# Kernel optimization log

Hardware: AMD Instinct MI355X
Metric: run time of the kernel (lower is better)

The kernel has to match this reference:

```python
import math
import jax, jax.numpy as jnp
import numpy as np

B, H, W, C = 2, 32, 32, 64
K = 15
G = 4
GC = C // G
K2 = K * K
RED = C // 4
MAX_SIGMA = 0.5


def setup_inputs() -> dict:
    key = jax.random.key(0)
    ks = jax.random.split(key, 32)
    f32 = jnp.float32

    def rn(k, shape, std):
        return (jax.random.normal(k, shape) * std).astype(f32)

    lin = 1.0 / math.sqrt(C)
    inp = {
        'x': jax.random.normal(ks[0], (B, H, W, C), f32),
        'raw_sigma': jnp.asarray(math.log(math.exp(0.3) - 1.0), f32),
        'base_offset_scale': jnp.asarray(0.1, f32),
        # input/output projections (stored [in,out])
        'w_ip': rn(ks[1], (C, C), lin), 'b_ip': jnp.zeros((C,), f32),
        'w_op': rn(ks[2], (C, C), lin), 'b_op': jnp.zeros((C,), f32),
        # dw_conv: depthwise 3x3 (HWIO, I=1) then pointwise 1x1 ([in,out])
        'w_dw': rn(ks[3], (3, 3, 1, C), 1.0 / 3.0), 'b_dw': jnp.zeros((C,), f32),
        'w_pw': rn(ks[4], (C, C), lin), 'b_pw': jnp.zeros((C,), f32),
        # offset / mask heads (original zero-inits; small random to exercise path)
        'w_off': rn(ks[5], (C, G * K2 * 2), 0.01), 'b_off': rn(ks[6], (G * K2 * 2,), 0.01),
        'w_msk': rn(ks[7], (C, G * K2), 0.01), 'b_msk': rn(ks[8], (G * K2,), 0.01),
        # kernel MLP: 2 -> 32 -> 32 -> G*GC
        'w_k1': rn(ks[9], (2, 32), 0.5), 'b_k1': jnp.zeros((32,), f32),
        'w_k2': rn(ks[10], (32, 32), 1.0 / math.sqrt(32)), 'b_k2': jnp.zeros((32,), f32),
        'w_k3': rn(ks[11], (32, G * GC), 1.0 / math.sqrt(32)), 'b_k3': jnp.zeros((G * GC,), f32),
        # SE block
        'w_fc1': rn(ks[12], (C, RED), lin), 'b_fc1': jnp.zeros((RED,), f32),
        'w_fc2': rn(ks[13], (RED, C), 1.0 / math.sqrt(RED)), 'b_fc2': jnp.zeros((C,), f32),
    }
    return inp


def _forward(x, raw_sigma, base_offset_scale, w_ip, b_ip, w_op, b_op, w_dw, b_dw,
             w_pw, b_pw, w_off, b_off, w_msk, b_msk, w_k1, b_k1, w_k2, b_k2,
             w_k3, b_k3, w_fc1, b_fc1, w_fc2, b_fc2):
    Bx, Hx, Wx, Cx = x.shape
    sigma = jnp.clip(jax.nn.softplus(raw_sigma), 1e-3, MAX_SIGMA)
    grid = jnp.linspace(-0.5, 0.5, K)  # [K]

    x_proj = x @ w_ip + b_ip  # [B,H,W,C]

    # depthwise 3x3 (SAME) + SiLU + pointwise 1x1
    y = jax.lax.conv_general_dilated(
        x, w_dw, (1, 1), 'SAME',
        dimension_numbers=('NHWC', 'HWIO', 'NHWC'), feature_group_count=Cx) + b_dw
    x_dw = jax.nn.silu(y) @ w_pw + b_pw  # [B,H,W,C]

    # Gaussian envelope over kernel grid, normalized
    env = jnp.exp(-(grid[:, None] ** 2 + grid[None, :] ** 2) / (2.0 * sigma ** 2))
    env = env / jnp.maximum(env.sum(), 1e-8)
    env_flat = env.reshape(1, 1, 1, 1, K2)

    gh, gw = jnp.meshgrid(grid, grid, indexing='ij')
    pos = jnp.stack([gh.ravel(), gw.ravel()], axis=-1) * 2.0  # [K2,2]
    hkw = jax.nn.silu(pos @ w_k1 + b_k1)
    hkw = jax.nn.silu(hkw @ w_k2 + b_k2)
    kw_raw = hkw @ w_k3 + b_k3  # [K2, G*GC]
    # faithful to torch view quirk: (K,K,G,gc) memory reinterpreted as (G,K2,gc)
    kw = kw_raw.reshape(G, K2, GC).reshape(1, 1, 1, G, K2, GC)

    offsets = (x_dw @ w_off + b_off).reshape(Bx, Hx, Wx, G, K2, 2) * base_offset_scale
    raw_mask = (x_dw @ w_msk + b_msk).reshape(Bx, Hx, Wx, G, K2) * env_flat
    attn = jnp.nan_to_num(jax.nn.softmax(raw_mask, axis=-1))

    # absolute sampling locations
    ref = jnp.linspace(-(K // 2), K // 2, K)
    rh, rw = jnp.meshgrid(ref, ref, indexing='ij')  # [K,K]
    pos_h = jnp.arange(Hx, dtype=x.dtype).reshape(1, Hx, 1, 1, 1)
    pos_w = jnp.arange(Wx, dtype=x.dtype).reshape(1, 1, Wx, 1, 1)
    abs_h = pos_h + rh.ravel().reshape(1, 1, 1, 1, K2) + offsets[..., 0]
    abs_w = pos_w + rw.ravel().reshape(1, 1, 1, 1, K2) + offsets[..., 1]
    ah = jnp.clip(abs_h, 0.0, Hx - 1)
    aw = jnp.clip(abs_w, 0.0, Wx - 1)
    h_f = jnp.clip(jnp.floor(ah).astype(jnp.int32), 0, Hx - 1)
    w_f = jnp.clip(jnp.floor(aw).astype(jnp.int32), 0, Wx - 1)
    h_c = jnp.minimum(h_f + 1, Hx - 1)
    w_c = jnp.minimum(w_f + 1, Wx - 1)
    hw = ah - h_f.astype(x.dtype)
    ww = aw - w_f.astype(x.dtype)
    valid = (~((abs_h < 0) | (abs_h > Hx - 1) | (abs_w < 0) | (abs_w > Wx - 1))).astype(x.dtype)

    xg = x_proj.reshape(Bx, Hx, Wx, G, GC)
    b_idx = jnp.arange(Bx).reshape(Bx, 1, 1, 1, 1)
    g_idx = jnp.arange(G).reshape(1, 1, 1, G, 1)
    v_ff = xg[b_idx, h_f, w_f, g_idx]  # [B,H,W,G,K2,GC]
    v_fc = xg[b_idx, h_f, w_c, g_idx]
    v_cf = xg[b_idx, h_c, w_f, g_idx]
    v_cc = xg[b_idx, h_c, w_c, g_idx]
    sampled = (v_ff * ((1 - hw) * (1 - ww) * valid)[..., None]
               + v_fc * ((1 - hw) * ww * valid)[..., None]
               + v_cf * (hw * (1 - ww) * valid)[..., None]
               + v_cc * (hw * ww * valid)[..., None])
    sampled = sampled * kw
    output = (sampled * attn[..., None]).sum(axis=4).reshape(Bx, Hx, Wx, Cx)

    # SE block (no mask, no bias)
    pooled = output.mean(axis=(1, 2), keepdims=True)
    se = jax.nn.silu(pooled @ w_fc1 + b_fc1) @ w_fc2 + b_fc2
    output = output * jax.nn.sigmoid(se)

    out = output @ w_op + b_op
    offset_reg = (offsets ** 2).mean()
    entropy = -(attn * jnp.log(attn + 1e-8)).sum(axis=-1).mean()
    return out, offset_reg, -entropy


def reference(x, raw_sigma, base_offset_scale, w_ip, b_ip, w_op, b_op, w_dw, b_dw,
              w_pw, b_pw, w_off, b_off, w_msk, b_msk, w_k1, b_k1, w_k2, b_k2,
              w_k3, b_k3, w_fc1, b_fc1, w_fc2, b_fc2):
    return _forward(x, raw_sigma, base_offset_scale, w_ip, b_ip, w_op, b_op,
                    w_dw, b_dw, w_pw, b_pw, w_off, b_off, w_msk, b_msk,
                    w_k1, b_k1, w_k2, b_k2, w_k3, b_k3, w_fc1, b_fc1, w_fc2, b_fc2)
```

## Files before the change

kernel.cpp:

```cpp
#include <hip/hip_runtime.h>
#include <math.h>

#define KK2 225
#define NPIX 2048
#define OFFC 1800
#define MSKC 900
#define NCOL 2700
#define NCOLP 2704

#define WROW 17
#define WCOL 20
#define WPOS (WROW*WCOL)
#define WSTR 68

#define WS_KW    0
#define WS_XPROJ 16384
#define WS_XDW   (16384+131072)
#define WS_OUT   (16384+2*131072)
#define WS_POOL  (16384+3*131072)
#define WS_GATE  (WS_POOL+128)
#define WS_ENTP  (WS_GATE+128)
#define WS_OFFP  (WS_ENTP+2048)
#define WS_PART2 (WS_OFFP+512)
#define WS_WB    (WS_PART2+4096)

typedef __attribute__((ext_vector_type(8))) short short8;
typedef __attribute__((ext_vector_type(4))) float f32x4;

__device__ __forceinline__ float silu(float a) { return a / (1.f + __expf(-a)); }
__device__ __forceinline__ unsigned short f2bf(float f) {
  unsigned u = __float_as_uint(f);
  u += 0x7FFFu + ((u >> 16) & 1u);
  return (unsigned short)(u >> 16);
}
__device__ __forceinline__ float bf2f(unsigned short h) {
  return __uint_as_float(((unsigned)h) << 16);
}

__global__ __launch_bounds__(256) void k_pre(
    const float* __restrict__ x,
    const float* __restrict__ w_ip, const float* __restrict__ b_ip,
    const float* __restrict__ w_dw, const float* __restrict__ b_dw,
    const float* __restrict__ w_pw, const float* __restrict__ b_pw,
    const float* __restrict__ w_k1, const float* __restrict__ b_k1,
    const float* __restrict__ w_k2, const float* __restrict__ b_k2,
    const float* __restrict__ w_k3, const float* __restrict__ b_k3,
    const float* __restrict__ w_off, const float* __restrict__ w_msk,
    float* __restrict__ ws)
{
  int t = threadIdx.x;
  if (blockIdx.x < 512) {
    int px = t >> 6, c = t & 63;
    int pix = blockIdx.x * 4 + px;
    int b = pix >> 10, h = (pix >> 5) & 31, w = pix & 31;
    __shared__ float xs[4][64], ys[4][64];
    xs[px][c] = x[pix*64 + c];
    float acc = b_dw[c];
    #pragma unroll
    for (int dh = -1; dh <= 1; dh++) {
      int hh = h + dh;
      if (hh < 0 || hh > 31) continue;
      #pragma unroll
      for (int dw2 = -1; dw2 <= 1; dw2++) {
        int wp = w + dw2;
        if (wp < 0 || wp > 31) continue;
        acc += x[(((b*32 + hh)*32 + wp) << 6) + c] * w_dw[((dh+1)*3 + (dw2+1))*64 + c];
      }
    }
    ys[px][c] = silu(acc);
    __syncthreads();
    float p1 = b_ip[c], p2 = b_pw[c];
    #pragma unroll 8
    for (int k = 0; k < 64; k++) {
      p1 += xs[px][k] * w_ip[k*64 + c];
      p2 += ys[px][k] * w_pw[k*64 + c];
    }
    ws[WS_XPROJ + pix*64 + c] = p1;
    ws[WS_XDW   + pix*64 + c] = p2;
  } else if (blockIdx.x < 569) {
    __shared__ float h1s[4][32], h2s[4][32];
    int tl = t >> 6, lane = t & 63;
    int tap = (blockIdx.x - 512) * 4 + tl;
    int tapc = min(tap, KK2 - 1);
    int i = tapc / 15, j = tapc % 15;
    float gi = -0.5f + (float)i * (1.0f/14.0f);
    float gj = -0.5f + (float)j * (1.0f/14.0f);
    float p0 = gi * 2.f, p1 = gj * 2.f;
    if (lane < 32) {
      float a = p0 * w_k1[lane] + p1 * w_k1[32 + lane] + b_k1[lane];
      h1s[tl][lane] = silu(a);
    }
    __syncthreads();
    if (lane < 32) {
      float a = b_k2[lane];
      #pragma unroll
      for (int q = 0; q < 32; q++) a += h1s[tl][q] * w_k2[q*32 + lane];
      h2s[tl][lane] = silu(a);
    }
    __syncthreads();
    float a = b_k3[lane];
    #pragma unroll
    for (int q = 0; q < 32; q++) a += h2s[tl][q] * w_k3[q*64 + lane];
    if (tap < KK2) ws[WS_KW + tap*64 + lane] = a;
  } else {
    unsigned short* wb = (unsigned short*)(ws + WS_WB);
    int cb = blockIdx.x - 569;
    int col = cb*16 + (t & 15);
    int kk = (t >> 4) * 4;
    unsigned short v4[4];
    #pragma unroll
    for (int j = 0; j < 4; j++) {
      int k = kk + j;
      float v = 0.f;
      if (col < OFFC)      v = w_off[k*OFFC + col];
      else if (col < NCOL) v = w_msk[k*MSKC + col - OFFC];
      v4[j] = f2bf(v);
    }
    *(uint2*)&wb[(size_t)col*64 + kk] = *(uint2*)v4;
  }
}

__global__ __launch_bounds__(1024, 8) void k_main(
    const float* __restrict__ raw_sigma,
    const float* __restrict__ base_scale,
    const float* __restrict__ b_off, const float* __restrict__ b_msk,
    float* __restrict__ ws)
{
  __shared__ unsigned short uni[WPOS*WSTR];
  __shared__ unsigned short off_s[4*OFFC];
  __shared__ float red_s[16];
  __shared__ float ent_sh[16];
  __shared__ float env_sum;

  unsigned short* xbs  = uni;
  unsigned short* mskr = uni + 1152;
  float* env_s = (float*)(uni + 4752);

  int t = threadIdx.x;
  int wv = t >> 6, lane = t & 63;
  int pix0 = blockIdx.x * 4;
  int b = pix0 >> 10;
  int h0 = (pix0 >> 5) & 31, w0 = pix0 & 31;
  const unsigned short* wb = (const unsigned short*)(ws + WS_WB);

  float sp = log1pf(__expf(raw_sigma[0]));
  float sigma = fminf(fmaxf(sp, 1e-3f), 0.5f);
  float envv = 0.f;
  if (t < KK2) {
    int i = t / 15, j = t % 15;
    float gi = -0.5f + (float)i * (1.0f/14.0f);
    float gj = -0.5f + (float)j * (1.0f/14.0f);
    envv = __expf(-(gi*gi + gj*gj) / (2.f*sigma*sigma));
  }
  if (t < 256) {
    int px = t >> 6, k = t & 63;
    xbs[px*72 + k] = f2bf(ws[WS_XDW + (pix0 + px)*64 + k]);
  } else if (t < 1024) {
    int r = t - 256;
    if (r < 768) {
      int px = 4 + (r >> 6), k = r & 63;
      xbs[px*72 + k] = 0;
    }
  }
  {
    float v = envv;
    #pragma unroll
    for (int m = 32; m > 0; m >>= 1) v += __shfl_xor(v, m);
    if (lane == 0) red_s[wv] = v;
    __syncthreads();
    if (t == 0) {
      float s = 0.f;
      #pragma unroll
      for (int q = 0; q < 16; q++) s += red_s[q];
      env_sum = fmaxf(s, 1e-8f);
    }
    __syncthreads();
    if (t < KK2) env_s[t] = envv / env_sum;
  }

  float scale = base_scale[0];
  float offreg = 0.f;
  int pxl = lane & 15;
  int rg = lane >> 4;
  int k0 = rg * 8;
  short8 bfrag_lo = *(const short8*)&xbs[pxl*72 + k0];
  short8 bfrag_hi = *(const short8*)&xbs[pxl*72 + k0 + 32];
  for (int tile = wv; tile < 169; tile += 16) {
    int col0 = tile * 16;
    int m = col0 + pxl;
    const short8 a_lo = *(const short8*)&wb[(size_t)m*64 + k0];
    const short8 a_hi = *(const short8*)&wb[(size_t)m*64 + k0 + 32];
    f32x4 acc = {0.f, 0.f, 0.f, 0.f};
    acc = __builtin_amdgcn_mfma_f32_16x16x32_bf16(a_lo, bfrag_lo, acc, 0, 0, 0);
    acc = __builtin_amdgcn_mfma_f32_16x16x32_bf16(a_hi, bfrag_hi, acc, 0, 0, 0);
    int cg = col0 + rg * 4;
    float4 bias;
    if (cg < OFFC) bias = *(const float4*)&b_off[cg];
    else           bias = *(const float4*)&b_msk[cg - OFFC];
    if (pxl < 4) {
      #pragma unroll
      for (int r = 0; r < 4; r++) {
        int col = cg + r;
        float val = acc[r] + ((const float*)&bias)[r];
        if (col < OFFC) {
          float o = val * scale;
          off_s[pxl*OFFC + col] = f2bf(o);
          offreg += o * o;
        } else if (col < NCOL) {
          mskr[pxl*MSKC + col - OFFC] = f2bf(val);
        }
      }
    }
  }
  {
    #pragma unroll
    for (int m = 32; m > 0; m >>= 1) offreg += __shfl_xor(offreg, m);
    __syncthreads();
    if (lane == 0) red_s[wv] = offreg;
    __syncthreads();
    if (t == 0) {
      float s = 0.f;
      #pragma unroll
      for (int q = 0; q < 16; q++) s += red_s[q];
      ws[WS_OFFP + blockIdx.x] = s;
    }
  }

  int spx = wv >> 2, g = wv & 3;
  float v[4];
  {
    float m = -INFINITY;
    #pragma unroll
    for (int kk = 0; kk < 4; kk++) {
      int p = lane + kk*64;
      if (p < KK2) { v[kk] = bf2f(mskr[spx*MSKC + g*KK2 + p]) * env_s[p]; m = fmaxf(m, v[kk]); }
      else v[kk] = -INFINITY;
    }
    #pragma unroll
    for (int s = 32; s > 0; s >>= 1) m = fmaxf(m, __shfl_xor(m, s));
    float sum = 0.f;
    #pragma unroll
    for (int kk = 0; kk < 4; kk++) {
      int p = lane + kk*64;
      if (p < KK2) { v[kk] = __expf(v[kk] - m); sum += v[kk]; }
    }
    #pragma unroll
    for (int s = 32; s > 0; s >>= 1) sum += __shfl_xor(sum, s);
    float inv = 1.f / sum;
    float ent = 0.f;
    #pragma unroll
    for (int kk = 0; kk < 4; kk++) {
      int p = lane + kk*64;
      if (p < KK2) {
        float a = v[kk] * inv;
        v[kk] = a;
        ent += a * __logf(a + 1e-8f);
      }
    }
    #pragma unroll
    for (int s = 32; s > 0; s >>= 1) ent += __shfl_xor(ent, s);
    if (lane == 0) ent_sh[wv] = ent;
  }
  __syncthreads();
  if (t < 4) ws[WS_ENTP + pix0 + t] =
      ent_sh[t*4] + ent_sh[t*4+1] + ent_sh[t*4+2] + ent_sh[t*4+3];

  {
    const float* xpb = ws + WS_XPROJ + (size_t)(b << 10)*64;
    for (int idx = t; idx < WPOS*8; idx += 1024) {
      int pos = idx >> 3, c8 = idx & 7;
      int r = pos / WCOL, c = pos - r*WCOL;
      int sh = min(max(h0 - 8 + r, 0), 31);
      int sw = min(max(w0 - 8 + c, 0), 31);
      const float* src = xpb + ((sh*32 + sw) << 6) + c8*8;
      float4 f0 = *(const float4*)src;
      float4 f1 = *(const float4*)(src + 4);
      uint2 u01, u23;
      u01.x = ((unsigned)f2bf(f0.y) << 16) | f2bf(f0.x);
      u01.y = ((unsigned)f2bf(f0.w) << 16) | f2bf(f0.z);
      u23.x = ((unsigned)f2bf(f1.y) << 16) | f2bf(f1.x);
      u23.y = ((unsigned)f2bf(f1.w) << 16) | f2bf(f1.z);
      *(uint2*)&uni[pos*WSTR + c8*8]     = u01;
      *(uint2*)&uni[pos*WSTR + c8*8 + 4] = u23;
    }
  }
  __syncthreads();

  {
    int ts = lane >> 2, cl = lane & 3;
    int wpx = w0 + spx;
    int chbase = g*16 + cl*4;
    const float* kwg = ws + WS_KW + g*3600 + cl*4;
    float4 acc = make_float4(0.f, 0.f, 0.f, 0.f);
    #pragma unroll
    for (int kq = 0; kq < 4; kq++) {
      float av = v[kq];
      int nIt = (kq == 3) ? 3 : 4;
      #pragma unroll 1
      for (int i2 = 0; i2 < nIt; i2++) {
        int p = kq*64 + i2*16 + ts;
        if (p < KK2) {
          float at = __shfl(av, i2*16 + ts);
          unsigned op = *(const unsigned*)&off_s[spx*OFFC + g*450 + p*2];
          float o0 = bf2f((unsigned short)(op & 0xFFFFu));
          float o1 = bf2f((unsigned short)(op >> 16));
          int pr = p / 15, pc = p - pr*15;
          float abs_h = (float)(h0 + pr - 7) + o0;
          float abs_w = (float)(wpx + pc - 7) + o1;
          float ah = fminf(fmaxf(abs_h, 0.f), 31.f);
          float aw = fminf(fmaxf(abs_w, 0.f), 31.f);
          int hf = (int)ah;
          int wf = (int)aw;
          float hw_ = ah - (float)hf, ww_ = aw - (float)wf;
          int rf = hf - h0 + 8;
          int rc = min(hf + 1, 31) - h0 + 8;
          int cf = wf - w0 + 8;
          int cc = min(wf + 1, 31) - w0 + 8;
          float s = (abs_h < 0.f || abs_h > 31.f || abs_w < 0.f || abs_w > 31.f) ? 0.f : at;
          float w00 = (1.f-hw_)*(1.f-ww_)*s, w01 = (1.f-hw_)*ww_*s;
          float w10 = hw_*(1.f-ww_)*s,       w11 = hw_*ww_*s;
          int rfb = rf*WSTR + chbase, rcb = rc*WSTR + chbase;
          uint2 qff = *(const uint2*)&uni[rfb + cf*WSTR*0 + cf* WSTR==0 ? 0 : 0];
          qff = *(const uint2*)&uni[(rf*WCOL + cf)*WSTR + chbase];
          uint2 qfc = *(const uint2*)&uni[(rf*WCOL + cc)*WSTR + chbase];
          uint2 qcf = *(const uint2*)&uni[(rc*WCOL + cf)*WSTR + chbase];
          uint2 qcc = *(const uint2*)&uni[(rc*WCOL + cc)*WSTR + chbase];
          float4 kwv = *(const float4*)&kwg[p*16];
          float ff0 = __uint_as_float(qff.x << 16), ff1 = __uint_as_float(qff.x & 0xFFFF0000u);
          float ff2 = __uint_as_float(qff.y << 16), ff3 = __uint_as_float(qff.y & 0xFFFF0000u);
          float fc0 = __uint_as_float(qfc.x << 16), fc1 = __uint_as_float(qfc.x & 0xFFFF0000u);
          float fc2 = __uint_as_float(qfc.y << 16), fc3 = __uint_as_float(qfc.y & 0xFFFF0000u);
          float cf0 = __uint_as_float(qcf.x << 16), cf1 = __uint_as_float(qcf.x & 0xFFFF0000u);
          float cf2 = __uint_as_float(qcf.y << 16), cf3 = __uint_as_float(qcf.y & 0xFFFF0000u);
          float cc0 = __uint_as_float(qcc.x << 16), cc1 = __uint_as_float(qcc.x & 0xFFFF0000u);
          float cc2 = __uint_as_float(qcc.y << 16), cc3 = __uint_as_float(qcc.y & 0xFFFF0000u);
          acc.x += (ff0*w00 + fc0*w01 + cf0*w10 + cc0*w11) * kwv.x;
          acc.y += (ff1*w00 + fc1*w01 + cf1*w10 + cc1*w11) * kwv.y;
          acc.z += (ff2*w00 + fc2*w01 + cf2*w10 + cc2*w11) * kwv.z;
          acc.w += (ff3*w00 + fc3*w01 + cf3*w10 + cc3*w11) * kwv.w;
        }
      }
    }
    #pragma unroll
    for (int m = 4; m < 64; m <<= 1) {
      acc.x += __shfl_xor(acc.x, m);
      acc.y += __shfl_xor(acc.y, m);
      acc.z += __shfl_xor(acc.z, m);
      acc.w += __shfl_xor(acc.w, m);
    }
    if (lane < 4) *(float4*)&ws[WS_OUT + (pix0 + spx)*64 + g*16 + cl*4] = acc;
  }
}

__global__ __launch_bounds__(256) void k_red(float* __restrict__ ws, float* __restrict__ d_out)
{
  __shared__ float red[256];
  int t = threadIdx.x, blk = blockIdx.x;
  if (blk < 64) {
    int b = blk >> 5, chunk = blk & 31;
    int c = t & 63, str = t >> 6;
    const float* base = ws + WS_OUT + (size_t)((b*1024 + chunk*32) << 6) + c;
    float s = 0.f;
    #pragma unroll
    for (int i = 0; i < 8; i++) s += base[((str + i*4) << 6)];
    red[t] = s;
    __syncthreads();
    if (t < 64) ws[WS_PART2 + blk*64 + t] =
      red[t] + red[t+64] + red[t+128] + red[t+192];
  } else if (blk == 64) {
    float s = 0.f;
    #pragma unroll
    for (int i = 0; i < 8; i++) s += ws[WS_ENTP + t + i*256];
    #pragma unroll
    for (int m = 32; m > 0; m >>= 1) s += __shfl_xor(s, m);
    if ((t & 63) == 0) red[t >> 6] = s;
    __syncthreads();
    if (t == 0) d_out[NPIX*64 + 1] = (red[0] + red[1] + red[2] + red[3]) * (1.f/8192.f);
  } else {
    float s = 0.f;
    #pragma unroll
    for (int i = 0; i < 2; i++) s += ws[WS_OFFP + t + i*256];
    #pragma unroll
    for (int m = 32; m > 0; m >>= 1) s += __shfl_xor(s, m);
    if ((t & 63) == 0) red[t >> 6] = s;
    __syncthreads();
    if (t == 0) d_out[NPIX*64] = (red[0] + red[1] + red[2] + red[3]) * (1.f/3686400.f);
  }
}

__global__ __launch_bounds__(128) void k_se(
    const float* __restrict__ w_fc1, const float* __restrict__ b_fc1,
    const float* __restrict__ w_fc2, const float* __restrict__ b_fc2,
    float* __restrict__ ws)
{
  __shared__ float pool_s[2][64];
  __shared__ float hsh[2][16];
  int t = threadIdx.x;
  int b = t >> 6, c = t & 63;
  {
    float s = 0.f;
    #pragma unroll
    for (int ch = 0; ch < 32; ch++) s += ws[WS_PART2 + (b*32 + ch)*64 + c];
    pool_s[b][c] = s * (1.f/1024.f);
  }
  __syncthreads();
  if (t < 32) {
    int bb = t >> 4, r = t & 15;
    float a = b_fc1[r];
    #pragma unroll 16
    for (int cc = 0; cc < 64; cc++) a += pool_s[bb][cc] * w_fc1[cc*16 + r];
    hsh[bb][r] = silu(a);
  }
  __syncthreads();
  float a = b_fc2[c];
  #pragma unroll
  for (int r = 0; r < 16; r++) a += hsh[b][r] * w_fc2[r*64 + c];
  ws[WS_GATE + b*64 + c] = 1.f / (1.f + __expf(-a));
}

__global__ __launch_bounds__(256) void k_final(
    const float* __restrict__ w_op, const float* __restrict__ b_op,
    const float* __restrict__ ws, float* __restrict__ d_out)
{
  int t = threadIdx.x;
  int px = t >> 6, c = t & 63;
  int pix = blockIdx.x * 4 + px;
  int b = pix >> 10;
  __shared__ float sc[4][64];
  sc[px][c] = ws[WS_OUT + pix*64 + c] * ws[WS_GATE + b*64 + c];
  __syncthreads();
  float a = b_op[c];
  #pragma unroll 8
  for (int k = 0; k < 64; k++) a += sc[px][k] * w_op[k*64 + c];
  d_out[pix*64 + c] = a;
}

extern "C" void kernel_launch(void* const* d_in, const int* in_sizes, int n_in,
                              void* d_out, int out_size, void* d_ws, size_t ws_size,
                              hipStream_t stream)
{
  const float* x     = (const float*)d_in[0];
  const float* rsig  = (const float*)d_in[1];
  const float* bos   = (const float*)d_in[2];
  const float* w_ip  = (const float*)d_in[3];
  const float* b_ip  = (const float*)d_in[4];
  const float* w_op  = (const float*)d_in[5];
  const float* b_op  = (const float*)d_in[6];
  const float* w_dw  = (const float*)d_in[7];
  const float* b_dw  = (const float*)d_in[8];
  const float* w_pw  = (const float*)d_in[9];
  const float* b_pw  = (const float*)d_in[10];
  const float* w_off = (const float*)d_in[11];
  const float* b_off = (const float*)d_in[12];
  const float* w_msk = (const float*)d_in[13];
  const float* b_msk = (const float*)d_in[14];
  const float* w_k1  = (const float*)d_in[15];
  const float* b_k1  = (const float*)d_in[16];
  const float* w_k2  = (const float*)d_in[17];
  const float* b_k2  = (const float*)d_in[18];
  const float* w_k3  = (const float*)d_in[19];
  const float* b_k3  = (const float*)d_in[20];
  const float* w_fc1 = (const float*)d_in[21];
  const float* b_fc1 = (const float*)d_in[22];
  const float* w_fc2 = (const float*)d_in[23];
  const float* b_fc2 = (const float*)d_in[24];
  float* ws  = (float*)d_ws;
  float* out = (float*)d_out;

  hipLaunchKernelGGL(k_pre, dim3(738), dim3(256), 0, stream,
                     x, w_ip, b_ip, w_dw, b_dw, w_pw, b_pw,
                     w_k1, b_k1, w_k2, b_k2, w_k3, b_k3, w_off, w_msk, ws);
  hipLaunchKernelGGL(k_main, dim3(512), dim3(1024), 0, stream,
                     rsig, bos, b_off, b_msk, ws);
  hipLaunchKernelGGL(k_red, dim3(66), dim3(256), 0, stream, ws, out);
  hipLaunchKernelGGL(k_se, dim3(1), dim3(128), 0, stream,
                     w_fc1, b_fc1, w_fc2, b_fc2, ws);
  hipLaunchKernelGGL(k_final, dim3(512), dim3(256), 0, stream,
                     w_op, b_op, ws, out);
}
```

Measured before the change: 61.25 us.

## Split offset/mask projection into standalone full-tile MFMA GEMM kernel

Moves the offset/mask head projection out of the fused sampling kernel into its own GEMM kernel. That kernel tiles 64 pixels by 64 columns, so every MFMA row carries a real pixel instead of only 4 of 16. This also stops each of the 512 sampling blocks from re-reading the full bf16 weight matrix. The head outputs now go to a bf16 buffer in the workspace, and the x_proj and dw-conv outputs are stored as bf16 so the window load becomes a direct copy. The offset regularizer is computed during sampling. In exchange it adds an extra kernel launch and a roughly 11 MB global write and read round trip.

```diff
diff --git a/kernel.cpp b/kernel.cpp
--- a/kernel.cpp
+++ b/kernel.cpp
@@ -7,6 +7,7 @@
 #define MSKC 900
 #define NCOL 2700
 #define NCOLP 2704
+#define HSTR 2704
 
 #define WROW 17
 #define WCOL 20
@@ -15,7 +16,7 @@
 
 #define WS_KW    0
 #define WS_XPROJ 16384
-#define WS_XDW   (16384+131072)
+#define WS_XB    (16384+131072)
 #define WS_OUT   (16384+2*131072)
 #define WS_POOL  (16384+3*131072)
 #define WS_GATE  (WS_POOL+128)
@@ -23,6 +24,7 @@
 #define WS_OFFP  (WS_ENTP+2048)
 #define WS_PART2 (WS_OFFP+512)
 #define WS_WB    (WS_PART2+4096)
+#define WS_HD    (WS_WB+86528)
 
 typedef __attribute__((ext_vector_type(8))) short short8;
 typedef __attribute__((ext_vector_type(4))) float f32x4;
@@ -75,8 +77,8 @@
       p1 += xs[px][k] * w_ip[k*64 + c];
       p2 += ys[px][k] * w_pw[k*64 + c];
     }
-    ws[WS_XPROJ + pix*64 + c] = p1;
-    ws[WS_XDW   + pix*64 + c] = p2;
+    ((unsigned short*)(ws + WS_XPROJ))[pix*64 + c] = f2bf(p1);
+    ((unsigned short*)(ws + WS_XB))[pix*64 + c]    = f2bf(p2);
   } else if (blockIdx.x < 569) {
     __shared__ float h1s[4][32], h2s[4][32];
     int tl = t >> 6, lane = t & 63;
@@ -120,28 +122,61 @@
   }
 }
 
-__global__ __launch_bounds__(1024, 8) void k_main(
-    const float* __restrict__ raw_sigma,
+__global__ __launch_bounds__(256) void k_gemm(
     const float* __restrict__ base_scale,
     const float* __restrict__ b_off, const float* __restrict__ b_msk,
     float* __restrict__ ws)
 {
+  int t = threadIdx.x;
+  int wv = t >> 6, lane = t & 63;
+  int row = lane & 15, rg = lane >> 4;
+  int k0 = rg * 8;
+  int colb = blockIdx.x * 64;
+  int pxb  = blockIdx.y * 64 + wv * 16;
+  const unsigned short* xb = (const unsigned short*)(ws + WS_XB);
+  const unsigned short* wb = (const unsigned short*)(ws + WS_WB);
+  unsigned short* hd = (unsigned short*)(ws + WS_HD);
+  float scale = base_scale[0];
+
+  short8 a_lo = *(const short8*)&xb[(size_t)(pxb + row)*64 + k0];
+  short8 a_hi = *(const short8*)&xb[(size_t)(pxb + row)*64 + k0 + 32];
+  #pragma unroll
+  for (int ct = 0; ct < 4; ct++) {
+    int c0 = colb + ct*16;
+    if (c0 >= NCOLP) break;
+    const short8 b_lo = *(const short8*)&wb[(size_t)(c0 + row)*64 + k0];
+    const short8 b_hi = *(const short8*)&wb[(size_t)(c0 + row)*64 + k0 + 32];
+    f32x4 acc = {0.f, 0.f, 0.f, 0.f};
+    acc = __builtin_amdgcn_mfma_f32_16x16x32_bf16(a_lo, b_lo, acc, 0, 0, 0);
+    acc = __builtin_amdgcn_mfma_f32_16x16x32_bf16(a_hi, b_hi, acc, 0, 0, 0);
+    int col = c0 + row;
+    float bias = 0.f, mult = 1.f;
+    if (col < OFFC)      { bias = b_off[col]; mult = scale; }
+    else if (col < NCOL) { bias = b_msk[col - OFFC]; }
+    #pragma unroll
+    for (int r = 0; r < 4; r++) {
+      int px = pxb + rg*4 + r;
+      hd[(size_t)px*HSTR + col] = f2bf((acc[r] + bias) * mult);
+    }
+  }
+}
+
+__global__ __launch_bounds__(1024, 8) void k_samp(
+    const float* __restrict__ raw_sigma,
+    float* __restrict__ ws)
+{
   __shared__ unsigned short uni[WPOS*WSTR];
-  __shared__ unsigned short off_s[4*OFFC];
+  __shared__ float env_s[KK2];
   __shared__ float red_s[16];
   __shared__ float ent_sh[16];
   __shared__ float env_sum;
-
-  unsigned short* xbs  = uni;
-  unsigned short* mskr = uni + 1152;
-  float* env_s = (float*)(uni + 4752);
 
   int t = threadIdx.x;
   int wv = t >> 6, lane = t & 63;
   int pix0 = blockIdx.x * 4;
   int b = pix0 >> 10;
   int h0 = (pix0 >> 5) & 31, w0 = pix0 & 31;
-  const unsigned short* wb = (const unsigned short*)(ws + WS_WB);
+  const unsigned short* hd = (const unsigned short*)(ws + WS_HD);
 
   float sp = log1pf(__expf(raw_sigma[0]));
   float sigma = fminf(fmaxf(sp, 1e-3f), 0.5f);
@@ -152,16 +187,6 @@
     float gj = -0.5f + (float)j * (1.0f/14.0f);
     envv = __expf(-(gi*gi + gj*gj) / (2.f*sigma*sigma));
   }
-  if (t < 256) {
-    int px = t >> 6, k = t & 63;
-    xbs[px*72 + k] = f2bf(ws[WS_XDW + (pix0 + px)*64 + k]);
-  } else if (t < 1024) {
-    int r = t - 256;
-    if (r < 768) {
-      int px = 4 + (r >> 6), k = r & 63;
-      xbs[px*72 + k] = 0;
-    }
-  }
   {
     float v = envv;
     #pragma unroll
@@ -178,62 +203,27 @@
     if (t < KK2) env_s[t] = envv / env_sum;
   }
 
-  float scale = base_scale[0];
-  float offreg = 0.f;
-  int pxl = lane & 15;
-  int rg = lane >> 4;
-  int k0 = rg * 8;
-  short8 bfrag_lo = *(const short8*)&xbs[pxl*72 + k0];
-  short8 bfrag_hi = *(const short8*)&xbs[pxl*72 + k0 + 32];
-  for (int tile = wv; tile < 169; tile += 16) {
-    int col0 = tile * 16;
-    int m = col0 + pxl;
-    const short8 a_lo = *(const short8*)&wb[(size_t)m*64 + k0];
-    const short8 a_hi = *(const short8*)&wb[(size_t)m*64 + k0 + 32];
-    f32x4 acc = {0.f, 0.f, 0.f, 0.f};
-    acc = __builtin_amdgcn_mfma_f32_16x16x32_bf16(a_lo, bfrag_lo, acc, 0, 0, 0);
-    acc = __builtin_amdgcn_mfma_f32_16x16x32_bf16(a_hi, bfrag_hi, acc, 0, 0, 0);
-    int cg = col0 + rg * 4;
-    float4 bias;
-    if (cg < OFFC) bias = *(const float4*)&b_off[cg];
-    else           bias = *(const float4*)&b_msk[cg - OFFC];
-    if (pxl < 4) {
-      #pragma unroll
-      for (int r = 0; r < 4; r++) {
-        int col = cg + r;
-        float val = acc[r] + ((const float*)&bias)[r];
-        if (col < OFFC) {
-          float o = val * scale;
-          off_s[pxl*OFFC + col] = f2bf(o);
-          offreg += o * o;
-        } else if (col < NCOL) {
-          mskr[pxl*MSKC + col - OFFC] = f2bf(val);
-        }
-      }
-    }
-  }
-  {
-    #pragma unroll
-    for (int m = 32; m > 0; m >>= 1) offreg += __shfl_xor(offreg, m);
-    __syncthreads();
-    if (lane == 0) red_s[wv] = offreg;
-    __syncthreads();
-    if (t == 0) {
-      float s = 0.f;
-      #pragma unroll
-      for (int q = 0; q < 16; q++) s += red_s[q];
-      ws[WS_OFFP + blockIdx.x] = s;
+  {
+    const unsigned short* xpb = (const unsigned short*)(ws + WS_XPROJ) + ((size_t)(b << 10) << 6);
+    for (int idx = t; idx < WPOS*16; idx += 1024) {
+      int pos = idx >> 4, c4 = idx & 15;
+      int r = pos / WCOL, c = pos - r*WCOL;
+      int sh = min(max(h0 - 8 + r, 0), 31);
+      int sw = min(max(w0 - 8 + c, 0), 31);
+      uint2 u = *(const uint2*)&xpb[((sh*32 + sw) << 6) + c4*4];
+      *(uint2*)&uni[pos*WSTR + c4*4] = u;
     }
   }
 
   int spx = wv >> 2, g = wv & 3;
+  const unsigned short* hrow = hd + (size_t)(pix0 + spx)*HSTR;
   float v[4];
   {
     float m = -INFINITY;
     #pragma unroll
     for (int kk = 0; kk < 4; kk++) {
       int p = lane + kk*64;
-      if (p < KK2) { v[kk] = bf2f(mskr[spx*MSKC + g*KK2 + p]) * env_s[p]; m = fmaxf(m, v[kk]); }
+      if (p < KK2) { v[kk] = bf2f(hrow[OFFC + g*KK2 + p]) * env_s[p]; m = fmaxf(m, v[kk]); }
       else v[kk] = -INFINITY;
     }
     #pragma unroll
@@ -265,27 +255,7 @@
   if (t < 4) ws[WS_ENTP + pix0 + t] =
       ent_sh[t*4] + ent_sh[t*4+1] + ent_sh[t*4+2] + ent_sh[t*4+3];
 
-  {
-    const float* xpb = ws + WS_XPROJ + (size_t)(b << 10)*64;
-    for (int idx = t; idx < WPOS*8; idx += 1024) {
-      int pos = idx >> 3, c8 = idx & 7;
-      int r = pos / WCOL, c = pos - r*WCOL;
-      int sh = min(max(h0 - 8 + r, 0), 31);
-      int sw = min(max(w0 - 8 + c, 0), 31);
-      const float* src = xpb + ((sh*32 + sw) << 6) + c8*8;
-      float4 f0 = *(const float4*)src;
-      float4 f1 = *(const float4*)(src + 4);
-      uint2 u01, u23;
-      u01.x = ((unsigned)f2bf(f0.y) << 16) | f2bf(f0.x);
-      u01.y = ((unsigned)f2bf(f0.w) << 16) | f2bf(f0.z);
-      u23.x = ((unsigned)f2bf(f1.y) << 16) | f2bf(f1.x);
-      u23.y = ((unsigned)f2bf(f1.w) << 16) | f2bf(f1.z);
-      *(uint2*)&uni[pos*WSTR + c8*8]     = u01;
-      *(uint2*)&uni[pos*WSTR + c8*8 + 4] = u23;
-    }
-  }
-  __syncthreads();
-
+  float offreg = 0.f;
   {
     int ts = lane >> 2, cl = lane & 3;
     int wpx = w0 + spx;
@@ -301,9 +271,10 @@
         int p = kq*64 + i2*16 + ts;
         if (p < KK2) {
           float at = __shfl(av, i2*16 + ts);
-          unsigned op = *(const unsigned*)&off_s[spx*OFFC + g*450 + p*2];
+          unsigned op = *(const unsigned*)&hrow[g*450 + p*2];
           float o0 = bf2f((unsigned short)(op & 0xFFFFu));
           float o1 = bf2f((unsigned short)(op >> 16));
+          if (cl == 0) offreg += o0*o0 + o1*o1;
           int pr = p / 15, pc = p - pr*15;
           float abs_h = (float)(h0 + pr - 7) + o0;
           float abs_w = (float)(wpx + pc - 7) + o1;
@@ -319,9 +290,7 @@
           float s = (abs_h < 0.f || abs_h > 31.f || abs_w < 0.f || abs_w > 31.f) ? 0.f : at;
           float w00 = (1.f-hw_)*(1.f-ww_)*s, w01 = (1.f-hw_)*ww_*s;
           float w10 = hw_*(1.f-ww_)*s,       w11 = hw_*ww_*s;
-          int rfb = rf*WSTR + chbase, rcb = rc*WSTR + chbase;
-          uint2 qff = *(const uint2*)&uni[rfb + cf*WSTR*0 + cf* WSTR==0 ? 0 : 0];
-          qff = *(const uint2*)&uni[(rf*WCOL + cf)*WSTR + chbase];
+          uint2 qff = *(const uint2*)&uni[(rf*WCOL + cf)*WSTR + chbase];
           uint2 qfc = *(const uint2*)&uni[(rf*WCOL + cc)*WSTR + chbase];
           uint2 qcf = *(const uint2*)&uni[(rc*WCOL + cf)*WSTR + chbase];
           uint2 qcc = *(const uint2*)&uni[(rc*WCOL + cc)*WSTR + chbase];
@@ -349,6 +318,18 @@
       acc.w += __shfl_xor(acc.w, m);
     }
     if (lane < 4) *(float4*)&ws[WS_OUT + (pix0 + spx)*64 + g*16 + cl*4] = acc;
+  }
+  {
+    #pragma unroll
+    for (int m = 32; m > 0; m >>= 1) offreg += __shfl_xor(offreg, m);
+    if (lane == 0) red_s[wv] = offreg;
+    __syncthreads();
+    if (t == 0) {
+      float s = 0.f;
+      #pragma unroll
+      for (int q = 0; q < 16; q++) s += red_s[q];
+      ws[WS_OFFP + blockIdx.x] = s;
+    }
   }
 }
 
@@ -470,8 +451,10 @@
   hipLaunchKernelGGL(k_pre, dim3(738), dim3(256), 0, stream,
                      x, w_ip, b_ip, w_dw, b_dw, w_pw, b_pw,
                      w_k1, b_k1, w_k2, b_k2, w_k3, b_k3, w_off, w_msk, ws);
-  hipLaunchKernelGGL(k_main, dim3(512), dim3(1024), 0, stream,
-                     rsig, bos, b_off, b_msk, ws);
+  hipLaunchKernelGGL(k_gemm, dim3(43, 32), dim3(256), 0, stream,
+                     bos, b_off, b_msk, ws);
+  hipLaunchKernelGGL(k_samp, dim3(512), dim3(1024), 0, stream,
+                     rsig, ws);
   hipLaunchKernelGGL(k_red, dim3(66), dim3(256), 0, stream, ws, out);
   hipLaunchKernelGGL(k_se, dim3(1), dim3(128), 0, stream,
                      w_fc1, b_fc1, w_fc2, b_fc2, ws);
```

Result: faster. 59.23 us (-3.3%).
